# Kernel optimization log

Measured on AMD Instinct MI355X. Metric: run time of the kernel, lower is better.

Reference implementation:

```python
import jax, jax.numpy as jnp
import numpy as np
from jax import lax

LATENT_DIM = 512
UNITS = LATENT_DIM // 2  # per-direction LSTM units (Keras LSTM(latent_dim//2))
FEAT = 512


def _lstm_scan(x, W, U, b):
    """Keras-style LSTM over x: [B, T, F]. Gate order i, f, g(candidate), o.
    Returns (hs [B,T,u], h_last [B,u], c_last [B,u])."""
    B = x.shape[0]
    u = U.shape[0]
    # Precompute input projections for all timesteps (one big GEMM).
    xz = jnp.einsum('btf,fg->btg', x, W) + b  # [B, T, 4u]

    def step(carry, zt):
        h, c = carry
        z = zt + h @ U  # [B, 4u]
        i = jax.nn.sigmoid(z[:, :u])
        f = jax.nn.sigmoid(z[:, u:2 * u])
        g = jnp.tanh(z[:, 2 * u:3 * u])
        o = jax.nn.sigmoid(z[:, 3 * u:])
        c_new = f * c + i * g
        h_new = o * jnp.tanh(c_new)
        return (h_new, c_new), h_new

    init = (jnp.zeros((B, u), x.dtype), jnp.zeros((B, u), x.dtype))
    (h_last, c_last), hs = lax.scan(step, init, jnp.swapaxes(xz, 0, 1))
    return jnp.swapaxes(hs, 0, 1), h_last, c_last


def setup_inputs() -> dict:
    key = jax.random.key(0)
    ks = jax.random.split(key, 7)
    B, T, F, u = 64, 1024, FEAT, UNITS
    s_in = 1.0 / np.sqrt(F)
    s_rec = 1.0 / np.sqrt(u)
    return {
        'x': jax.random.normal(ks[0], (B, T, F), jnp.float32),
        'W_fwd': jax.random.normal(ks[1], (F, 4 * u), jnp.float32) * s_in,
        'U_fwd': jax.random.normal(ks[2], (u, 4 * u), jnp.float32) * s_rec,
        'b_fwd': jnp.zeros((4 * u,), jnp.float32),
        'W_bwd': jax.random.normal(ks[3], (F, 4 * u), jnp.float32) * s_in,
        'U_bwd': jax.random.normal(ks[4], (u, 4 * u), jnp.float32) * s_rec,
        'b_bwd': jnp.zeros((4 * u,), jnp.float32),
    }


def reference(x, W_fwd, U_fwd, b_fwd, W_bwd, U_bwd, b_bwd):
    # Forward direction
    hs_f, h_f, c_f = _lstm_scan(x, W_fwd, U_fwd, b_fwd)
    # Backward direction: process reversed sequence, re-reverse outputs (Keras Bidirectional)
    hs_b, h_b, c_b = _lstm_scan(x[:, ::-1, :], W_bwd, U_bwd, b_bwd)
    hs_b = hs_b[:, ::-1, :]
    enc_out = jnp.concatenate([hs_f, hs_b], axis=-1)  # [B, T, latent]
    h = jnp.concatenate([h_f, h_b], axis=-1)          # [B, latent]
    c = jnp.concatenate([c_f, c_b], axis=-1)          # [B, latent]
    return enc_out, h, c
```

## Files before the change

### kernel.cpp

```cpp
#include <hip/hip_runtime.h>
#include <cstdint>
#include <cstddef>

typedef _Float16 f16x2 __attribute__((ext_vector_type(2)));
typedef _Float16 half4 __attribute__((ext_vector_type(4)));
typedef _Float16 half8 __attribute__((ext_vector_type(8)));
typedef float f32x4 __attribute__((ext_vector_type(4)));

static constexpr int BB = 64;
static constexpr int TT = 1024;
static constexpr int FF = 512;
static constexpr int UU = 256;
static constexpr int NZ = 1024;

static constexpr size_t LSTM_SHBYTES = 90112;
static constexpr int HREP_STRIDE = 608;

__device__ __forceinline__ f16x2 bc16(unsigned int v) { return __builtin_bit_cast(f16x2, v); }

__device__ __forceinline__ void st_u32_rlx(unsigned int* p, unsigned int v)
{
    __hip_atomic_store(p, v, __ATOMIC_RELAXED, __HIP_MEMORY_SCOPE_AGENT);
}
__device__ __forceinline__ unsigned int ld_u32_rlx(const unsigned int* p)
{
    return __hip_atomic_load(p, __ATOMIC_RELAXED, __HIP_MEMORY_SCOPE_AGENT);
}

__device__ __forceinline__ void bar_lgkm()
{
    asm volatile("s_waitcnt lgkmcnt(0)\n\ts_barrier" ::: "memory");
}

__device__ __forceinline__ float qsum(float v)
{
    int b1 = __builtin_amdgcn_mov_dpp(__builtin_bit_cast(int, v), 0xB1, 0xf, 0xf, true);
    v += __builtin_bit_cast(float, b1);
    int b2 = __builtin_amdgcn_mov_dpp(__builtin_bit_cast(int, v), 0x4E, 0xf, 0xf, true);
    v += __builtin_bit_cast(float, b2);
    return v;
}

__global__ __launch_bounds__(256) void enc_cast_x(
    const float* __restrict__ x, _Float16* __restrict__ x16, int n4)
{
    int stride = gridDim.x * 256;
    for (int i = blockIdx.x * 256 + threadIdx.x; i < n4; i += stride) {
        float4 v = ((const float4*)x)[i];
        half4 o;
        o.x = (_Float16)v.x; o.y = (_Float16)v.y;
        o.z = (_Float16)v.z; o.w = (_Float16)v.w;
        ((half4*)x16)[i] = o;
    }
}

__global__ __launch_bounds__(256) void enc_cast_wt(
    const float* __restrict__ Wf, const float* __restrict__ Wb,
    _Float16* __restrict__ WT)
{
    __shared__ float tile[64][65];
    const int t = threadIdx.x;
    const int k0 = blockIdx.x * 64;
    const int n0 = blockIdx.y * 64;
    const int d = blockIdx.z;
    const float* W = d ? Wb : Wf;
    _Float16* WTd = WT + (size_t)d * NZ * FF;
#pragma unroll
    for (int p = 0; p < 16; ++p) {
        int idx = p * 256 + t;
        int r = idx >> 6, c = idx & 63;
        tile[r][c] = W[(size_t)(k0 + r) * NZ + n0 + c];
    }
    __syncthreads();
#pragma unroll
    for (int p = 0; p < 16; ++p) {
        int idx = p * 256 + t;
        int r = idx >> 6, c = idx & 63;
        WTd[(size_t)(n0 + r) * FF + k0 + c] = (_Float16)tile[c][r];
    }
}

__global__ __launch_bounds__(256) void enc_pack_u16v2(
    const float* __restrict__ Uf, const float* __restrict__ Ub,
    uint4* __restrict__ Upkr2)
{
    int idx = blockIdx.x * 256 + threadIdx.x;
    if (idx >= 2 * 128 * 256) return;
    int d  = idx >> 15;
    int k2 = (idx >> 8) & 127;
    int j  = idx & 255;
    int k = 2 * k2;
    const float* Ud = d ? Ub : Uf;
    unsigned int w[4];
#pragma unroll
    for (int g = 0; g < 4; ++g) {
        f16x2 h;
        h.x = (_Float16)Ud[(size_t)k * NZ + g * 256 + j];
        h.y = (_Float16)Ud[(size_t)(k + 1) * NZ + g * 256 + j];
        w[g] = __builtin_bit_cast(unsigned int, h);
    }
    Upkr2[idx] = make_uint4(w[0], w[1], w[2], w[3]);
}

__global__ __launch_bounds__(256) void enc_zero(float* __restrict__ p, int n)
{
    int i = blockIdx.x * 256 + threadIdx.x;
    if (i < n) p[i] = 0.f;
}

__global__ __launch_bounds__(256) void enc_gemm16(
    const _Float16* __restrict__ x16, const _Float16* __restrict__ WT,
    const float* __restrict__ bf, const float* __restrict__ bb,
    _Float16* __restrict__ xz16, int c0, int CT)
{
    __shared__ __align__(16) _Float16 Ash[128][40];
    __shared__ __align__(16) _Float16 Bsh[128][40];

    const int t = threadIdx.x;
    const int r0 = blockIdx.x * 128;
    const int n0 = blockIdx.y * 128;
    const int MperD = BB * CT;
    const int d = r0 / MperD;

    const int srow = t >> 2;
    const int koff = (t & 3) * 8;

    auto xrowptr = [&](int r) -> const _Float16* {
        int rd = r - d * MperD;
        int b = rd / CT;
        int tl = rd - b * CT;
        int tsrc = d ? (TT - 1 - (c0 + tl)) : (c0 + tl);
        return x16 + ((size_t)b * TT + tsrc) * FF;
    };
    const _Float16* ap0 = xrowptr(r0 + srow);
    const _Float16* ap1 = xrowptr(r0 + 64 + srow);
    const _Float16* wp0 = WT + (size_t)(d * NZ + n0 + srow) * FF;
    const _Float16* wp1 = wp0 + (size_t)64 * FF;

    const int lane = t & 63;
    const int w = t >> 6;
    const int wm = w >> 1, wn = w & 1;
    const int l15 = lane & 15;
    const int kq = (lane >> 4) * 8;

    f32x4 acc[4][4];
#pragma unroll
    for (int i = 0; i < 4; ++i)
#pragma unroll
        for (int j = 0; j < 4; ++j) acc[i][j] = (f32x4)0.f;

    for (int ks = 0; ks < FF / 32; ++ks) {
        const int k0 = ks * 32;
        uint4 av0 = *(const uint4*)(ap0 + k0 + koff);
        uint4 av1 = *(const uint4*)(ap1 + k0 + koff);
        uint4 bv0 = *(const uint4*)(wp0 + k0 + koff);
        uint4 bv1 = *(const uint4*)(wp1 + k0 + koff);
        __syncthreads();
        *(uint4*)&Ash[srow][koff]      = av0;
        *(uint4*)&Ash[64 + srow][koff] = av1;
        *(uint4*)&Bsh[srow][koff]      = bv0;
        *(uint4*)&Bsh[64 + srow][koff] = bv1;
        __syncthreads();

        half8 af[4], bfr[4];
#pragma unroll
        for (int mf = 0; mf < 4; ++mf)
            af[mf] = *(const half8*)&Ash[wm * 64 + mf * 16 + l15][kq];
#pragma unroll
        for (int nf = 0; nf < 4; ++nf)
            bfr[nf] = *(const half8*)&Bsh[wn * 64 + nf * 16 + l15][kq];
#pragma unroll
        for (int mf = 0; mf < 4; ++mf)
#pragma unroll
            for (int nf = 0; nf < 4; ++nf)
                acc[mf][nf] = __builtin_amdgcn_mfma_f32_16x16x32_f16(
                    af[mf], bfr[nf], acc[mf][nf], 0, 0, 0);
    }

    const float* bd = d ? bb : bf;
    const int rbase = r0 + wm * 64;
    const int cbase = n0 + wn * 64;
#pragma unroll
    for (int nf = 0; nf < 4; ++nf) {
        const int cc = cbase + nf * 16 + l15;
        const float bia = bd[cc];
#pragma unroll
        for (int mf = 0; mf < 4; ++mf) {
#pragma unroll
            for (int rg = 0; rg < 4; ++rg) {
                int rr = rbase + mf * 16 + (lane >> 4) * 4 + rg;
                xz16[(size_t)rr * NZ + cc] = (_Float16)(acc[mf][nf][rg] + bia);
            }
        }
    }
}

template <int MBASE>
__device__ __forceinline__ void dot16(const uint4 (&ureg)[32], const char* hptr,
                                      float& a0, float& a1, float& a2, float& a3)
{
#pragma unroll
    for (int r = 0; r < 4; ++r) {
        uint4 hq = *(const uint4*)(hptr + r * 16);
#pragma unroll
        for (int e = 0; e < 4; ++e) {
            f16x2 hw = bc16((&hq.x)[e]);
            const uint4 uv = ureg[MBASE + r * 4 + e];
            a0 = __builtin_amdgcn_fdot2(hw, bc16(uv.x), a0, false);
            a1 = __builtin_amdgcn_fdot2(hw, bc16(uv.y), a1, false);
            a2 = __builtin_amdgcn_fdot2(hw, bc16(uv.z), a2, false);
            a3 = __builtin_amdgcn_fdot2(hw, bc16(uv.w), a3, false);
        }
    }
}

__device__ __forceinline__ float sigm_f(float xv)
{
    return 1.0f / (1.0f + __expf(-xv));
}
__device__ __forceinline__ float tanh_f(float xv)
{
    return 2.0f / (1.0f + __expf(-2.0f * xv)) - 1.0f;
}

__global__ __launch_bounds__(512, 2) void enc_lstm_quad(
    const _Float16* __restrict__ xz16, const uint4* __restrict__ Upkr2,
    float* __restrict__ hstate, float* __restrict__ cstate,
    unsigned int* __restrict__ hbuf,
    float* __restrict__ out, int c0, int CT)
{
    extern __shared__ char smem2[];

    const int t  = threadIdx.x;
    const int q  = t & 3;
    const int jl = t >> 2;
    const int w  = t >> 6;
    const int beta = blockIdx.x;
    const int jh = beta >> 7;
    const int c  = beta & 127;
    const int d  = c >> 6;
    const int b  = c & 63;
    const int j  = jh * 128 + jl;
    const int partner = beta ^ 128;

    const uint4* Uq = Upkr2 + (size_t)d * 128 * 256 + j;
    uint4 ureg[32];
#pragma unroll
    for (int m = 0; m < 16; ++m)
        ureg[m] = Uq[(size_t)(q * 16 + m) * 256];
#pragma unroll
    for (int m = 0; m < 16; ++m)
        ureg[16 + m] = Uq[(size_t)(64 + q * 16 + m) * 256];

    float cr = cstate[(size_t)c * UU + j];
    float hn = 0.f;
    if (t < 256) {
        _Float16 hv = (_Float16)hstate[(size_t)c * UU + t];
        *(unsigned short*)(smem2 + ((t & 127) >> 5) * HREP_STRIDE + t * 2) =
            __builtin_bit_cast(unsigned short, hv);
    }
    __syncthreads();

    const _Float16* xzrow = xz16 + (size_t)c * CT * NZ;
    float* outb = out + (size_t)b * TT * (2 * UU) + d * UU;

    const char* hp0 = smem2 + q * HREP_STRIDE + (0 * 16 + q * 4) * 16;
    const char* hp1 = smem2 + q * HREP_STRIDE + (1 * 16 + q * 4) * 16;

    const int al = t - 384;
    const int pj = (1 - jh) * 128 + (al & 127);
    unsigned int pref = 0;

    for (int tl = 0; tl < CT; ++tl) {
        const int step = c0 + tl + 1;
        const int htag = c0 + tl;

        const unsigned short xq =
            *((const unsigned short*)(xzrow + (size_t)tl * NZ) + q * 256 + j);

        if (w >= 6 && tl > 0) {
            const unsigned int* pp =
                &hbuf[((size_t)(htag & 1) * 256 + partner) * 128 + al];
            unsigned int v = pref;
            while ((v >> 16) != (unsigned int)htag)
                v = ld_u32_rlx(pp);
            *(unsigned short*)(smem2 + (al >> 5) * HREP_STRIDE + pj * 2) =
                (unsigned short)(v & 0xffffu);
        }

        float a0 = 0.f, a1 = 0.f, a2 = 0.f, a3 = 0.f;
        if (jh == 0) dot16<0>(ureg, hp0, a0, a1, a2, a3);
        else         dot16<16>(ureg, hp1, a0, a1, a2, a3);
        bar_lgkm();

        if (jh == 0) dot16<16>(ureg, hp1, a0, a1, a2, a3);
        else         dot16<0>(ureg, hp0, a0, a1, a2, a3);

        {
            float xv = (float)__builtin_bit_cast(_Float16, xq);
            a0 += (q == 0) ? xv : 0.f;
            a1 += (q == 1) ? xv : 0.f;
            a2 += (q == 2) ? xv : 0.f;
            a3 += (q == 3) ? xv : 0.f;
        }
        float zi = qsum(a0), zf = qsum(a1), zg = qsum(a2), zo = qsum(a3);

        float ig = sigm_f(zi), fg = sigm_f(zf), gg = tanh_f(zg), og = sigm_f(zo);
        cr = fg * cr + ig * gg;
        hn = og * tanh_f(cr);
        _Float16 h16 = (_Float16)hn;
        unsigned short hbits = __builtin_bit_cast(unsigned short, h16);

        if (q == 0) {
            st_u32_rlx(&hbuf[((size_t)(step & 1) * 256 + beta) * 128 + jl],
                       ((unsigned int)step << 16) | (unsigned int)hbits);
            int tsrc = d ? (TT - 1 - (c0 + tl)) : (c0 + tl);
            outb[(size_t)tsrc * (2 * UU) + j] = hn;
            *(unsigned short*)(smem2 + (jl >> 5) * HREP_STRIDE + j * 2) = hbits;
        }
        if (w >= 6) {
            pref = ld_u32_rlx(
                &hbuf[((size_t)(step & 1) * 256 + partner) * 128 + al]);
        }
        bar_lgkm();
    }

    if (q == 0) {
        hstate[(size_t)c * UU + j] = hn;
        cstate[(size_t)c * UU + j] = cr;
    }
}

__global__ __launch_bounds__(256) void enc_final(
    const float* __restrict__ hstate, const float* __restrict__ cstate,
    float* __restrict__ out)
{
    int idx = blockIdx.x * 256 + threadIdx.x;
    if (idx >= 2 * BB * UU) return;
    int d = idx / (BB * UU);
    int rem = idx - d * (BB * UU);
    int b = rem / UU;
    int j = rem - b * UU;
    size_t OUT_H = (size_t)BB * TT * (2 * UU);
    size_t HSZ = (size_t)BB * (2 * UU);
    out[OUT_H + (size_t)b * (2 * UU) + d * UU + j] = hstate[idx];
    out[OUT_H + HSZ + (size_t)b * (2 * UU) + d * UU + j] = cstate[idx];
}

extern "C" void kernel_launch(void* const* d_in, const int* in_sizes, int n_in,
                              void* d_out, int out_size, void* d_ws, size_t ws_size,
                              hipStream_t stream)
{
    const float* x  = (const float*)d_in[0];
    const float* Wf = (const float*)d_in[1];
    const float* Uf = (const float*)d_in[2];
    const float* bf = (const float*)d_in[3];
    const float* Wb = (const float*)d_in[4];
    const float* Ub = (const float*)d_in[5];
    const float* bb = (const float*)d_in[6];
    float* out = (float*)d_out;

    const size_t x16_bytes   = (size_t)BB * TT * FF * 2;
    const size_t wt_bytes    = (size_t)2 * NZ * FF * 2;
    const size_t upk_bytes   = (size_t)2 * 128 * 256 * sizeof(uint4);
    const size_t state_bytes = (size_t)2 * BB * UU * sizeof(float);
    const size_t hbuf_bytes  = (size_t)2 * 256 * 128 * 4;
    const size_t fixed = x16_bytes + wt_bytes + upk_bytes + 2 * state_bytes
                       + hbuf_bytes;

    int CT = TT;
    while (CT > 8) {
        size_t need = fixed + (size_t)2 * BB * CT * NZ * 2;
        if (need <= ws_size) break;
        CT >>= 1;
    }

    char* wsb = (char*)d_ws;
    _Float16* x16 = (_Float16*)wsb;
    _Float16* WT  = (_Float16*)(wsb + x16_bytes);
    uint4* Upkr2  = (uint4*)(wsb + x16_bytes + wt_bytes);
    float* hstate = (float*)(wsb + x16_bytes + wt_bytes + upk_bytes);
    float* cstate = hstate + 2 * BB * UU;
    unsigned int* hbuf = (unsigned int*)(wsb + x16_bytes + wt_bytes + upk_bytes
                                         + 2 * state_bytes);
    _Float16* xz16 = (_Float16*)(wsb + fixed);

    (void)hipFuncSetAttribute(reinterpret_cast<const void*>(enc_lstm_quad),
                              hipFuncAttributeMaxDynamicSharedMemorySize,
                              (int)LSTM_SHBYTES);

    enc_cast_x<<<4096, 256, 0, stream>>>(x, x16, BB * TT * FF / 4);
    enc_cast_wt<<<dim3(8, 16, 2), 256, 0, stream>>>(Wf, Wb, WT);
    enc_pack_u16v2<<<(2 * 128 * 256 + 255) / 256, 256, 0, stream>>>(Uf, Ub, Upkr2);
    enc_zero<<<(2 * 2 * BB * UU + 255) / 256, 256, 0, stream>>>(hstate, 2 * 2 * BB * UU);

    for (int c0 = 0; c0 < TT; c0 += CT) {
        dim3 ggrid((2 * BB * CT) / 128, NZ / 128);
        enc_gemm16<<<ggrid, 256, 0, stream>>>(x16, WT, bf, bb, xz16, c0, CT);
        enc_lstm_quad<<<256, 512, LSTM_SHBYTES, stream>>>(
            xz16, Upkr2, hstate, cstate, hbuf, out, c0, CT);
    }
    enc_final<<<(2 * BB * UU + 255) / 256, 256, 0, stream>>>(hstate, cstate, out);
}
```

Baseline: 1.751 ms.

## Run each LSTM sequence in one 1024-thread block, splitting U across registers, LDS and L2

Result: slower. 2.377 ms (+35.8%).

```diff
diff --git a/kernel.cpp b/kernel.cpp
--- a/kernel.cpp
+++ b/kernel.cpp
@@ -13,19 +13,13 @@
 static constexpr int UU = 256;
 static constexpr int NZ = 1024;
 
-static constexpr size_t LSTM_SHBYTES = 90112;
-static constexpr int HREP_STRIDE = 608;
+static constexpr int UREG = 20;
+static constexpr int ULDS = 8;
+static constexpr size_t ULDS_BYTES = (size_t)ULDS * 1024 * 16;
+static constexpr size_t H_SECT = 144;
+static constexpr size_t LSTM_SHBYTES = ULDS_BYTES + 1024;
 
 __device__ __forceinline__ f16x2 bc16(unsigned int v) { return __builtin_bit_cast(f16x2, v); }
-
-__device__ __forceinline__ void st_u32_rlx(unsigned int* p, unsigned int v)
-{
-    __hip_atomic_store(p, v, __ATOMIC_RELAXED, __HIP_MEMORY_SCOPE_AGENT);
-}
-__device__ __forceinline__ unsigned int ld_u32_rlx(const unsigned int* p)
-{
-    return __hip_atomic_load(p, __ATOMIC_RELAXED, __HIP_MEMORY_SCOPE_AGENT);
-}
 
 __device__ __forceinline__ void bar_lgkm()
 {
@@ -195,25 +189,6 @@
     }
 }
 
-template <int MBASE>
-__device__ __forceinline__ void dot16(const uint4 (&ureg)[32], const char* hptr,
-                                      float& a0, float& a1, float& a2, float& a3)
-{
-#pragma unroll
-    for (int r = 0; r < 4; ++r) {
-        uint4 hq = *(const uint4*)(hptr + r * 16);
-#pragma unroll
-        for (int e = 0; e < 4; ++e) {
-            f16x2 hw = bc16((&hq.x)[e]);
-            const uint4 uv = ureg[MBASE + r * 4 + e];
-            a0 = __builtin_amdgcn_fdot2(hw, bc16(uv.x), a0, false);
-            a1 = __builtin_amdgcn_fdot2(hw, bc16(uv.y), a1, false);
-            a2 = __builtin_amdgcn_fdot2(hw, bc16(uv.z), a2, false);
-            a3 = __builtin_amdgcn_fdot2(hw, bc16(uv.w), a3, false);
-        }
-    }
-}
-
 __device__ __forceinline__ float sigm_f(float xv)
 {
     return 1.0f / (1.0f + __expf(-xv));
@@ -223,78 +198,86 @@
     return 2.0f / (1.0f + __expf(-2.0f * xv)) - 1.0f;
 }
 
-__global__ __launch_bounds__(512, 2) void enc_lstm_quad(
+__global__ __launch_bounds__(1024) void enc_lstm_full(
     const _Float16* __restrict__ xz16, const uint4* __restrict__ Upkr2,
     float* __restrict__ hstate, float* __restrict__ cstate,
-    unsigned int* __restrict__ hbuf,
     float* __restrict__ out, int c0, int CT)
 {
     extern __shared__ char smem2[];
-
-    const int t  = threadIdx.x;
-    const int q  = t & 3;
-    const int jl = t >> 2;
-    const int w  = t >> 6;
-    const int beta = blockIdx.x;
-    const int jh = beta >> 7;
-    const int c  = beta & 127;
-    const int d  = c >> 6;
-    const int b  = c & 63;
-    const int j  = jh * 128 + jl;
-    const int partner = beta ^ 128;
-
-    const uint4* Uq = Upkr2 + (size_t)d * 128 * 256 + j;
-    uint4 ureg[32];
-#pragma unroll
-    for (int m = 0; m < 16; ++m)
-        ureg[m] = Uq[(size_t)(q * 16 + m) * 256];
-#pragma unroll
-    for (int m = 0; m < 16; ++m)
-        ureg[16 + m] = Uq[(size_t)(64 + q * 16 + m) * 256];
+    uint4* ulds = (uint4*)smem2;
+    char*  hbase = smem2 + ULDS_BYTES;
+
+    const int t = threadIdx.x;
+    const int q = t & 3;
+    const int j = t >> 2;
+    const int c = blockIdx.x;
+    const int d = c >> 6;
+    const int b = c & 63;
+    const int jq4 = t;
+
+    const uint4* Uq = Upkr2 + ((size_t)d * 128 + q * 32) * 256 + j;
+    uint4 ureg[UREG];
+#pragma unroll
+    for (int m = 0; m < UREG; ++m) ureg[m] = Uq[(size_t)m * 256];
+#pragma unroll
+    for (int m = 0; m < ULDS; ++m)
+        ulds[(size_t)m * 1024 + jq4] = Uq[(size_t)(UREG + m) * 256];
+    const uint4* Ul2 = Uq + (size_t)(UREG + ULDS) * 256;
 
     float cr = cstate[(size_t)c * UU + j];
     float hn = 0.f;
     if (t < 256) {
         _Float16 hv = (_Float16)hstate[(size_t)c * UU + t];
-        *(unsigned short*)(smem2 + ((t & 127) >> 5) * HREP_STRIDE + t * 2) =
+        *(unsigned short*)(hbase + (t >> 6) * H_SECT + (t & 63) * 2) =
             __builtin_bit_cast(unsigned short, hv);
     }
     __syncthreads();
 
     const _Float16* xzrow = xz16 + (size_t)c * CT * NZ;
     float* outb = out + (size_t)b * TT * (2 * UU) + d * UU;
-
-    const char* hp0 = smem2 + q * HREP_STRIDE + (0 * 16 + q * 4) * 16;
-    const char* hp1 = smem2 + q * HREP_STRIDE + (1 * 16 + q * 4) * 16;
-
-    const int al = t - 384;
-    const int pj = (1 - jh) * 128 + (al & 127);
-    unsigned int pref = 0;
+    const char* hrd = hbase + q * H_SECT;
+
+    unsigned short xq = *((const unsigned short*)xzrow + q * 256 + j);
 
     for (int tl = 0; tl < CT; ++tl) {
-        const int step = c0 + tl + 1;
-        const int htag = c0 + tl;
-
-        const unsigned short xq =
-            *((const unsigned short*)(xzrow + (size_t)tl * NZ) + q * 256 + j);
-
-        if (w >= 6 && tl > 0) {
-            const unsigned int* pp =
-                &hbuf[((size_t)(htag & 1) * 256 + partner) * 128 + al];
-            unsigned int v = pref;
-            while ((v >> 16) != (unsigned int)htag)
-                v = ld_u32_rlx(pp);
-            *(unsigned short*)(smem2 + (al >> 5) * HREP_STRIDE + pj * 2) =
-                (unsigned short)(v & 0xffffu);
-        }
+        uint4 u28 = Ul2[0];
+        uint4 u29 = Ul2[256];
+        uint4 u30 = Ul2[512];
+        uint4 u31 = Ul2[768];
 
         float a0 = 0.f, a1 = 0.f, a2 = 0.f, a3 = 0.f;
-        if (jh == 0) dot16<0>(ureg, hp0, a0, a1, a2, a3);
-        else         dot16<16>(ureg, hp1, a0, a1, a2, a3);
-        bar_lgkm();
-
-        if (jh == 0) dot16<16>(ureg, hp1, a0, a1, a2, a3);
-        else         dot16<0>(ureg, hp0, a0, a1, a2, a3);
+        auto dotw = [&](const uint4& uv, unsigned int hw) {
+            f16x2 h2 = bc16(hw);
+            a0 = __builtin_amdgcn_fdot2(h2, bc16(uv.x), a0, false);
+            a1 = __builtin_amdgcn_fdot2(h2, bc16(uv.y), a1, false);
+            a2 = __builtin_amdgcn_fdot2(h2, bc16(uv.z), a2, false);
+            a3 = __builtin_amdgcn_fdot2(h2, bc16(uv.w), a3, false);
+        };
+
+#pragma unroll
+        for (int r = 0; r < 5; ++r) {
+            uint4 hq = *(const uint4*)(hrd + r * 16);
+            dotw(ureg[4 * r + 0], hq.x);
+            dotw(ureg[4 * r + 1], hq.y);
+            dotw(ureg[4 * r + 2], hq.z);
+            dotw(ureg[4 * r + 3], hq.w);
+        }
+#pragma unroll
+        for (int r = 5; r < 7; ++r) {
+            uint4 hq = *(const uint4*)(hrd + r * 16);
+#pragma unroll
+            for (int e = 0; e < 4; ++e) {
+                uint4 uv = ulds[(size_t)(4 * (r - 5) + e) * 1024 + jq4];
+                dotw(uv, (&hq.x)[e]);
+            }
+        }
+        {
+            uint4 hq = *(const uint4*)(hrd + 7 * 16);
+            dotw(u28, hq.x);
+            dotw(u29, hq.y);
+            dotw(u30, hq.z);
+            dotw(u31, hq.w);
+        }
 
         {
             float xv = (float)__builtin_bit_cast(_Float16, xq);
@@ -308,19 +291,19 @@
         float ig = sigm_f(zi), fg = sigm_f(zf), gg = tanh_f(zg), og = sigm_f(zo);
         cr = fg * cr + ig * gg;
         hn = og * tanh_f(cr);
-        _Float16 h16 = (_Float16)hn;
-        unsigned short hbits = __builtin_bit_cast(unsigned short, h16);
-
+        unsigned short hbits =
+            __builtin_bit_cast(unsigned short, (_Float16)hn);
+
+        {
+            int tn = (tl + 1 < CT) ? tl + 1 : tl;
+            xq = *((const unsigned short*)(xzrow + (size_t)tn * NZ) + q * 256 + j);
+        }
+
+        bar_lgkm();
         if (q == 0) {
-            st_u32_rlx(&hbuf[((size_t)(step & 1) * 256 + beta) * 128 + jl],
-                       ((unsigned int)step << 16) | (unsigned int)hbits);
+            *(unsigned short*)(hbase + (j >> 6) * H_SECT + (j & 63) * 2) = hbits;
             int tsrc = d ? (TT - 1 - (c0 + tl)) : (c0 + tl);
             outb[(size_t)tsrc * (2 * UU) + j] = hn;
-            *(unsigned short*)(smem2 + (jl >> 5) * HREP_STRIDE + j * 2) = hbits;
-        }
-        if (w >= 6) {
-            pref = ld_u32_rlx(
-                &hbuf[((size_t)(step & 1) * 256 + partner) * 128 + al]);
         }
         bar_lgkm();
     }
@@ -364,9 +347,7 @@
     const size_t wt_bytes    = (size_t)2 * NZ * FF * 2;
     const size_t upk_bytes   = (size_t)2 * 128 * 256 * sizeof(uint4);
     const size_t state_bytes = (size_t)2 * BB * UU * sizeof(float);
-    const size_t hbuf_bytes  = (size_t)2 * 256 * 128 * 4;
-    const size_t fixed = x16_bytes + wt_bytes + upk_bytes + 2 * state_bytes
-                       + hbuf_bytes;
+    const size_t fixed = x16_bytes + wt_bytes + upk_bytes + 2 * state_bytes;
 
     int CT = TT;
     while (CT > 8) {
@@ -381,11 +362,9 @@
     uint4* Upkr2  = (uint4*)(wsb + x16_bytes + wt_bytes);
     float* hstate = (float*)(wsb + x16_bytes + wt_bytes + upk_bytes);
     float* cstate = hstate + 2 * BB * UU;
-    unsigned int* hbuf = (unsigned int*)(wsb + x16_bytes + wt_bytes + upk_bytes
-                                         + 2 * state_bytes);
     _Float16* xz16 = (_Float16*)(wsb + fixed);
 
-    (void)hipFuncSetAttribute(reinterpret_cast<const void*>(enc_lstm_quad),
+    (void)hipFuncSetAttribute(reinterpret_cast<const void*>(enc_lstm_full),
                               hipFuncAttributeMaxDynamicSharedMemorySize,
                               (int)LSTM_SHBYTES);
 
@@ -397,8 +376,8 @@
     for (int c0 = 0; c0 < TT; c0 += CT) {
         dim3 ggrid((2 * BB * CT) / 128, NZ / 128);
         enc_gemm16<<<ggrid, 256, 0, stream>>>(x16, WT, bf, bb, xz16, c0, CT);
-        enc_lstm_quad<<<256, 512, LSTM_SHBYTES, stream>>>(
-            xz16, Upkr2, hstate, cstate, hbuf, out, c0, CT);
+        enc_lstm_full<<<128, 1024, LSTM_SHBYTES, stream>>>(
+            xz16, Upkr2, hstate, cstate, out, c0, CT);
     }
     enc_final<<<(2 * BB * UU + 255) / 256, 256, 0, stream>>>(hstate, cstate, out);
 }
```
